# Kernel optimization log

Measured on AMD Instinct MI355X. Metric: run time of the kernel, lower is better.

The kernel has to match this reference:

```python
import jax, jax.numpy as jnp
import numpy as np

N, C, H, W = 4, 256, 60, 60
CIMG = 5  # rgb/ir channels after add_position (3 + x + y)
K = 8
ITERS = 2


def setup_inputs() -> dict:
    key = jax.random.key(0)
    ks = jax.random.split(key, 12)
    inp = {
        "cnn_encoder_output": jax.random.normal(ks[0], (N, C, H, W), jnp.float32),
        "rgb": jax.random.normal(ks[1], (N, CIMG, H, W), jnp.float32),
        "ir": jax.random.normal(ks[2], (N, CIMG, H, W), jnp.float32),
        # g-MLP (mlp_num_layers=1): Linear(2C -> C), torch weight layout [out, in]
        "W_g_rgb": jax.random.normal(ks[3], (C, 2 * C), jnp.float32) * 0.02,
        "b_g_rgb": jnp.zeros((C,), jnp.float32),
        "W_g_ir": jax.random.normal(ks[4], (C, 2 * C), jnp.float32) * 0.02,
        "b_g_ir": jnp.zeros((C,), jnp.float32),
        # SE block: Linear(2C -> C//16) -> ReLU -> Linear(C//16 -> C) -> Sigmoid
        "W_se1": jax.random.normal(ks[5], (C // 16, 2 * C), jnp.float32) * 0.02,
        "b_se1": jnp.zeros((C // 16,), jnp.float32),
        "W_se2": jax.random.normal(ks[6], (C, C // 16), jnp.float32) * 0.02,
        "b_se2": jnp.zeros((C,), jnp.float32),
        "gamma": jnp.ones((1,), jnp.float32),
        "gnn_iterations": ITERS,
        "k": K,
    }
    return inp


def _knn_indices(x, k):
    # x: [N, HW, D] -> indices of k nearest neighbours [N, HW, k]
    r = jnp.einsum("nid,njd->nij", x, x)          # gram matrix
    sq = jnp.einsum("nid,nid->ni", x, x)          # squared norms
    d2 = sq[:, :, None] + sq[:, None, :] - 2.0 * r
    d = jnp.sqrt(jnp.maximum(d2, 0.0))
    d = jax.lax.stop_gradient(d)
    _, idx = jax.lax.top_k(-d, k)                  # smallest distances
    return idx


def _gather(h, idx):
    # h: [N, HW, C], idx: [N, HW, K] -> [N, HW, K, C]
    return jax.vmap(lambda hn, i: hn[i])(h, idx)


def reference(cnn_encoder_output, rgb, ir, W_g_rgb, b_g_rgb, W_g_ir, b_g_ir,
              W_se1, b_se1, W_se2, b_se2, gamma, gnn_iterations, k):
    n, c, hh, ww = cnn_encoder_output.shape
    hw = hh * ww
    rgb_f = rgb.reshape(n, rgb.shape[1], hw).transpose(0, 2, 1)  # [N, HW, 5]
    ir_f = ir.reshape(n, ir.shape[1], hw).transpose(0, 2, 1)
    knn_rgb = _knn_indices(rgb_f, k)  # [N, HW, K]
    knn_ir = _knn_indices(ir_f, k)

    h = cnn_encoder_output.transpose(0, 2, 3, 1).reshape(n, hw, c)  # [N, HW, C]

    for _ in range(gnn_iterations):
        rgb_nb = _gather(h, knn_rgb)  # [N, HW, K, C]
        ir_nb = _gather(h, knn_ir)
        rgb_feat = jnp.concatenate([rgb_nb, rgb_nb - ir_nb], axis=-1)  # [N,HW,K,2C]
        ir_feat = jnp.concatenate([ir_nb, ir_nb - rgb_nb], axis=-1)
        m_rgb = jnp.max(jax.nn.relu(jnp.einsum("nhkf,cf->nhkc", rgb_feat, W_g_rgb) + b_g_rgb), axis=2)
        m_ir = jnp.max(jax.nn.relu(jnp.einsum("nhkf,cf->nhkc", ir_feat, W_g_ir) + b_g_ir), axis=2)
        cc = jnp.concatenate([m_rgb, m_ir], axis=-1).mean(axis=1, keepdims=True)  # [N,1,2C]
        se = jax.nn.sigmoid(jax.nn.relu(cc @ W_se1.T + b_se1) @ W_se2.T + b_se2)  # [N,1,C]
        h = se * h

    h = h.reshape(n, hh, ww, c).transpose(0, 3, 1, 2)
    return jax.nn.relu(gamma * h + cnn_encoder_output)
```

## Files before the change

kernel.cpp:

```cpp
#include <hip/hip_runtime.h>
#include <hip/hip_bf16.h>

#define NB 4
#define CH 256
#define HWT 3600
#define KNN 8
#define POSB 16
#define MPAD 3712

#define SSEGP 8
#define CAND 450
#define PAIRS 225
#define ROWS3 450

#define GEMM_BLKS 928

typedef __attribute__((ext_vector_type(8))) __bf16 bf16x8;
typedef __attribute__((ext_vector_type(4))) float f32x4;
typedef __attribute__((ext_vector_type(2))) float f32x2;
typedef __attribute__((ext_vector_type(2))) unsigned u32x2;
typedef __attribute__((ext_vector_type(4))) unsigned u32x4;

__device__ inline float med3f(float a, float b, float c) {
    return __builtin_amdgcn_fmed3f(a, b, c);
}

__device__ __forceinline__ void insert8(float* best, float kf) {
    best[7] = med3f(best[6], best[7], kf);
    best[6] = med3f(best[5], best[6], kf);
    best[5] = med3f(best[4], best[5], kf);
    best[4] = med3f(best[3], best[4], kf);
    best[3] = med3f(best[2], best[3], kf);
    best[2] = med3f(best[1], best[2], kf);
    best[1] = med3f(best[0], best[1], kf);
    best[0] = fminf(best[0], kf);
}


__device__ __forceinline__ void gemm_body(int lid, int n,
                                          const __hip_bfloat16* __restrict__ Abf,
                                          const __hip_bfloat16* __restrict__ Wbf,
                                          __hip_bfloat16* __restrict__ Yall,
                                          char* smem) {
    char* sA = smem;
    char* sB = smem + 16384;
    int w = (lid & 7) * 29 + (lid >> 3);
    int m0 = (w >> 3) * 128;
    int o0 = (w & 7) * 128;
    int t = threadIdx.x;
    int lane = t & 63, wid = t >> 6;
    int wm = wid >> 1, wo = wid & 1;

    const __hip_bfloat16* Ab = Abf + (size_t)n * MPAD * CH;
    const __hip_bfloat16* Wb = Wbf + (size_t)n * 1024 * CH;

    f32x4 acc[4][4] = {};

    int srow = t >> 3;
    int sslot = t & 7;
    int swz = (sslot ^ (srow & 7)) << 4;
    int fr = lane & 15;
    int kg = lane >> 4;
    int p = lane & 7;

    uint4 av[4], bv[4];
    auto load_tile = [&](int ks) {
#pragma unroll
        for (int r = 0; r < 4; ++r) {
            int row = srow + 32 * r;
            av[r] = *(const uint4*)(Ab + ((size_t)(m0 + row)) * CH + ks * 64 + sslot * 8);
            bv[r] = *(const uint4*)(Wb + ((size_t)(o0 + row)) * CH + ks * 64 + sslot * 8);
        }
    };
    load_tile(0);

    for (int ks = 0; ks < 4; ++ks) {
        __syncthreads();
#pragma unroll
        for (int r = 0; r < 4; ++r) {
            int row = srow + 32 * r;
            *(uint4*)(sA + row * 128 + swz) = av[r];
            *(uint4*)(sB + row * 128 + swz) = bv[r];
        }
        __syncthreads();
        if (ks < 3) load_tile(ks + 1);
#pragma unroll
        for (int kk = 0; kk < 2; ++kk) {
            bf16x8 hf[4], wf[4];
            int slot = kk * 4 + kg;
            int inrow = (slot ^ p) << 4;
#pragma unroll
            for (int f = 0; f < 4; ++f) {
                hf[f] = *(const bf16x8*)(sA + (wm * 64 + f * 16 + fr) * 128 + inrow);
                wf[f] = *(const bf16x8*)(sB + (wo * 64 + f * 16 + fr) * 128 + inrow);
            }
#pragma unroll
            for (int fa = 0; fa < 4; ++fa)
#pragma unroll
                for (int fb = 0; fb < 4; ++fb)
                    acc[fa][fb] = __builtin_amdgcn_mfma_f32_16x16x32_bf16(
                        wf[fa], hf[fb], acc[fa][fb], 0, 0, 0);
        }
    }

    __syncthreads();
#pragma unroll
    for (int fa = 0; fa < 4; ++fa)
#pragma unroll
        for (int fb = 0; fb < 4; ++fb) {
            int ml = wm * 64 + fb * 16 + fr;
            int ob = (wo * 64 + fa * 16 + kg * 4) * 2;
            f32x4 v = acc[fa][fb];
            union { ushort4 u; __hip_bfloat16 h[4]; } pk;
            pk.h[0] = __float2bfloat16(v.x);
            pk.h[1] = __float2bfloat16(v.y);
            pk.h[2] = __float2bfloat16(v.z);
            pk.h[3] = __float2bfloat16(v.w);
            int swzb = (ob & ~15) ^ ((ml & 15) << 4);
            *(ushort4*)(smem + ml * 256 + swzb + (ob & 15)) = pk.u;
        }
    __syncthreads();
    __hip_bfloat16* Y = Yall + (size_t)n * HWT * 1024;
    int colb = (t & 15) * 16;
#pragma unroll
    for (int i = 0; i < 8; ++i) {
        int row = i * 16 + (t >> 4);
        int grow = m0 + row;
        if (grow < HWT) {
            u32x4 v = *(const u32x4*)(smem + row * 256 + (colb ^ ((row & 15) << 4)));
            __builtin_nontemporal_store(v, (u32x4*)((char*)Y + (size_t)grow * 2048 + o0 * 2 + colb));
        }
    }
}

__global__ __launch_bounds__(256) void gemm_k(const __hip_bfloat16* __restrict__ Abf,
                                              const __hip_bfloat16* __restrict__ Wbf,
                                              __hip_bfloat16* __restrict__ Yall) {
    __shared__ char smem[32768];
    int gid = blockIdx.x;
    gemm_body(gid % 232, gid / 232, Abf, Wbf, Yall, smem);
}

__global__ __launch_bounds__(256) void knn_main(const float* __restrict__ xpack,
                                                unsigned* __restrict__ partial) {
    int seg = blockIdx.x, rb = blockIdx.y, nm = blockIdx.z;
    int t = threadIdx.x;
    const float* xp = xpack + (size_t)nm * HWT * 8;
    __shared__ f32x2 xs[PAIRS * 6];

    if (t < PAIRS) {
        int j = seg * CAND + 2 * t;
        float4 a0 = ((const float4*)xp)[(size_t)j * 2];
        float4 b0 = ((const float4*)xp)[(size_t)j * 2 + 1];
        float4 a1 = ((const float4*)xp)[(size_t)(j + 1) * 2];
        float4 b1 = ((const float4*)xp)[(size_t)(j + 1) * 2 + 1];
        f32x2* o = xs + t * 6;
        o[0] = f32x2{a0.x, a1.x};
        o[1] = f32x2{a0.y, a1.y};
        o[2] = f32x2{a0.z, a1.z};
        o[3] = f32x2{a0.w, a1.w};
        o[4] = f32x2{b0.x, b1.x};
        o[5] = f32x2{b0.y + 1.0f, b1.y + 1.0f};
    }
    __syncthreads();

    bool active = (t < PAIRS);
    int r0 = rb * ROWS3 + t;
    int rr0 = active ? r0 : 0;
    int rr1 = active ? (r0 + PAIRS) : 0;
    float4 a0 = ((const float4*)xp)[(size_t)rr0 * 2];
    float4 b0 = ((const float4*)xp)[(size_t)rr0 * 2 + 1];
    float4 a1 = ((const float4*)xp)[(size_t)rr1 * 2];
    float4 b1 = ((const float4*)xp)[(size_t)rr1 * 2 + 1];
    f32x2 q01 = f32x2{b0.y, b0.y};
    f32x2 q11 = f32x2{b1.y, b1.y};

    const float BIG = __uint_as_float(0x7F000000u);
    float bst0[8], bst1[8];
#pragma unroll
    for (int i = 0; i < 8; ++i) { bst0[i] = BIG; bst1[i] = BIG; }

    unsigned jg0 = (unsigned)(seg * CAND);
#pragma unroll 3
    for (int p = 0; p < PAIRS; ++p) {
        f32x2 cx = xs[p * 6 + 0];
        f32x2 cy = xs[p * 6 + 1];
        f32x2 cz = xs[p * 6 + 2];
        f32x2 cw = xs[p * 6 + 3];
        f32x2 cv = xs[p * 6 + 4];
        f32x2 cq = xs[p * 6 + 5];
        f32x2 d0 = cx * a0.x;
        d0 += cy * a0.y;
        d0 += cz * a0.z;
        d0 += cw * a0.w;
        d0 += cv * b0.x;
        f32x2 s0 = cq + q01;
        f32x2 e0 = s0 - 2.0f * d0;
        f32x2 d1 = cx * a1.x;
        d1 += cy * a1.y;
        d1 += cz * a1.z;
        d1 += cw * a1.w;
        d1 += cv * b1.x;
        f32x2 s1 = cq + q11;
        f32x2 e1 = s1 - 2.0f * d1;

        unsigned jA = jg0 + 2 * p, jB = jA + 1;
        u32x2 u0, u1;
        __builtin_memcpy(&u0, &e0, 8);
        __builtin_memcpy(&u1, &e1, 8);
        insert8(bst0, __uint_as_float((u0.x & 0xFFFFF000u) | jA));
        insert8(bst0, __uint_as_float((u0.y & 0xFFFFF000u) | jB));
        insert8(bst1, __uint_as_float((u1.x & 0xFFFFF000u) | jA));
        insert8(bst1, __uint_as_float((u1.y & 0xFFFFF000u) | jB));
    }
    if (active) {
        unsigned* o = partial + (((size_t)(nm * SSEGP + seg)) * HWT + r0) * 8;
        ((uint4*)o)[0] = uint4{ __float_as_uint(bst0[0]), __float_as_uint(bst0[1]),
                                __float_as_uint(bst0[2]), __float_as_uint(bst0[3]) };
        ((uint4*)o)[1] = uint4{ __float_as_uint(bst0[4]), __float_as_uint(bst0[5]),
                                __float_as_uint(bst0[6]), __float_as_uint(bst0[7]) };
        unsigned* o1 = partial + (((size_t)(nm * SSEGP + seg)) * HWT + r0 + PAIRS) * 8;
        ((uint4*)o1)[0] = uint4{ __float_as_uint(bst1[0]), __float_as_uint(bst1[1]),
                                 __float_as_uint(bst1[2]), __float_as_uint(bst1[3]) };
        ((uint4*)o1)[1] = uint4{ __float_as_uint(bst1[4]), __float_as_uint(bst1[5]),
                                 __float_as_uint(bst1[6]), __float_as_uint(bst1[7]) };
    }
}

__global__ __launch_bounds__(256) void fusedA(const float* __restrict__ cnn,
                                              __hip_bfloat16* __restrict__ Abf,
                                              const float* __restrict__ Wg_rgb,
                                              const float* __restrict__ Wg_ir,
                                              float* __restrict__ Wcomb,
                                              float* __restrict__ g,
                                              __hip_bfloat16* __restrict__ Wbf,
                                              const float* __restrict__ rgb,
                                              const float* __restrict__ ir,
                                              float* __restrict__ xpack) {
    int bid = blockIdx.x;
    int t = threadIdx.x;
    if (bid < GEMM_BLKS) {
        __shared__ float st[64][65];
        int n = bid / 232;
        int rem = bid - n * 232;
        int k0 = (rem / 58) * 64;
        int m0 = (rem % 58) * 64;
        const float* src = cnn + (size_t)n * CH * HWT;
#pragma unroll
        for (int r = 0; r < 4; ++r) {
            int kl = r * 16 + (t >> 4);
            int ms = (t & 15) * 4;
            float4 v = {0.f, 0.f, 0.f, 0.f};
            if (m0 + ms < HWT) v = *(const float4*)(src + (size_t)(k0 + kl) * HWT + m0 + ms);
            st[ms + 0][kl] = v.x; st[ms + 1][kl] = v.y;
            st[ms + 2][kl] = v.z; st[ms + 3][kl] = v.w;
        }
        __syncthreads();
        int m = t >> 2, kg = (t & 3) * 16;
        union { uint4 u[2]; __hip_bfloat16 h[16]; } pk;
#pragma unroll
        for (int i = 0; i < 16; ++i) pk.h[i] = __float2bfloat16(st[m][kg + i]);
        __hip_bfloat16* dst = Abf + ((size_t)n * MPAD + m0 + m) * CH + k0 + kg;
        ((uint4*)dst)[0] = pk.u[0];
        ((uint4*)dst)[1] = pk.u[1];
    } else if (bid < GEMM_BLKS + 1024) {
        int e = (bid - GEMM_BLKS) * 256 + t;
        int o = e >> 8, j = e & 255;
        float v;
        if (o < 256)      v = Wg_rgb[o * 512 + j] + Wg_rgb[o * 512 + 256 + j];
        else if (o < 512) v = Wg_rgb[(o - 256) * 512 + 256 + j];
        else if (o < 768) v = Wg_ir[(o - 512) * 512 + j] + Wg_ir[(o - 512) * 512 + 256 + j];
        else              v = Wg_ir[(o - 768) * 512 + 256 + j];
        Wcomb[e] = v;
        __hip_bfloat16 h = __float2bfloat16(v);
#pragma unroll
        for (int n = 0; n < NB; ++n) Wbf[(size_t)n * 262144 + e] = h;
        if (e < NB * CH) g[e] = 1.0f;
    } else {
        int e = (bid - GEMM_BLKS - 1024) * 256 + t;
        if (e < 2 * NB * HWT) {
            int nm = e / HWT, j = e - nm * HWT;
            int mod = nm / NB, n = nm - mod * NB;
            const float* x = (mod == 0 ? rgb : ir) + (size_t)n * 5 * HWT;
            float v[5], q = 0.f;
#pragma unroll
            for (int d = 0; d < 5; ++d) { v[d] = x[d * HWT + j]; q = fmaf(v[d], v[d], q); }
            float* o = xpack + (size_t)e * 8;
#pragma unroll
            for (int d = 0; d < 5; ++d) o[d] = v[d];
            o[5] = q; o[6] = 0.f; o[7] = 0.f;
        }
    }
}

__global__ __launch_bounds__(256) void knn_merge_zero(const unsigned* __restrict__ partial,
                                                      int* __restrict__ knn_rgb,
                                                      int* __restrict__ knn_ir,
                                                      float* __restrict__ ccsum) {
    int bid = blockIdx.x;
    if (bid >= 450) {
        int e = (bid - 450) * 256 + threadIdx.x;
        if (e < NB * 512) ccsum[e] = 0.f;
        return;
    }
    int tid = bid * 256 + threadIdx.x;
    int rid = tid >> 1, sub = tid & 1;
    int nm = rid / HWT, row = rid - nm * HWT;
    const float BIG = __uint_as_float(0x7F000000u);
    float best[8];
#pragma unroll
    for (int i = 0; i < 8; ++i) best[i] = BIG;
    for (int s = sub; s < SSEGP; s += 2) {
        const unsigned* p = partial + (((size_t)(nm * SSEGP + s)) * HWT + row) * 8;
#pragma unroll
        for (int w = 0; w < 2; ++w) {
            uint4 v = ((const uint4*)p)[w];
            unsigned vv[4] = { v.x, v.y, v.z, v.w };
#pragma unroll
            for (int e = 0; e < 4; ++e) insert8(best, __uint_as_float(vv[e]));
        }
    }
    float other[8];
#pragma unroll
    for (int i = 0; i < 8; ++i) other[i] = __shfl_xor(best[i], 1);
#pragma unroll
    for (int i = 0; i < 8; ++i) insert8(best, other[i]);
    if (sub == 0) {
        int mod = nm / NB, n = nm - mod * NB;
        int* o = (mod == 0 ? knn_rgb : knn_ir) + ((size_t)n * HWT + row) * KNN;
#pragma unroll
        for (int i = 0; i < 8; ++i) o[i] = (int)(__float_as_uint(best[i]) & 0xFFFu);
    }
}

__global__ __launch_bounds__(256) void scale_w_zero(const float* __restrict__ Wcomb,
                                                    const float* __restrict__ g,
                                                    __hip_bfloat16* __restrict__ Wbf,
                                                    float* __restrict__ ccsum) {
    int bid = blockIdx.x;
    if (bid >= 512) {
        int e = (bid - 512) * 256 + threadIdx.x;
        if (e < NB * 512) ccsum[e] = 0.f;
        return;
    }
    int n = bid >> 7;
    int gid = (bid & 127) * 256 + threadIdx.x;
    int o = gid >> 5;
    int kb = (gid & 31) * 8;
    const float* w = Wcomb + o * 256 + kb;
    const float* gp = g + n * CH + kb;
    union { uint4 u; __hip_bfloat16 h[8]; } pk;
#pragma unroll
    for (int i = 0; i < 8; ++i) pk.h[i] = __float2bfloat16(w[i] * gp[i]);
    *(uint4*)(Wbf + ((size_t)n * 1024 + o) * CH + kb) = pk.u;
}

__global__ __launch_bounds__(256) void gather_kernel(const __hip_bfloat16* __restrict__ Yall,
                                                     const int* __restrict__ knn_rgb,
                                                     const int* __restrict__ knn_ir,
                                                     const float* __restrict__ b_rgb,
                                                     const float* __restrict__ b_ir,
                                                     float* __restrict__ ccsum) {
    int lid = blockIdx.x;
    int xcd = lid & 7, sub = lid >> 3;
    int wg = (xcd < 4 ? xcd * 113 : 4 * 113 + (xcd - 4) * 112) + sub;
    int n = wg / 225;
    int hwbase = (wg - n * 225) * POSB;
    int t = threadIdx.x;
    int half = t >> 7;
    int cp = (t & 127) << 1;
    __shared__ int sidx[POSB][2][KNN];
    {
        int p = t >> 4, rem = t & 15;
        int hw = hwbase + p;
        int v;
        if (rem < 8) v = knn_rgb[((size_t)n * HWT + hw) * KNN + rem];
        else         v = knn_ir[((size_t)n * HWT + hw) * KNN + (rem - 8)];
        sidx[p][rem >> 3][rem & 7] = v;
    }
    __syncthreads();
    const float* bias = half ? b_ir : b_rgb;
    float b0 = bias[cp], b1 = bias[cp + 1];
    float acc0 = 0.f, acc1 = 0.f;
    const __hip_bfloat16* Y = Yall + (size_t)n * HWT * 1024;
    int offA = half * 512 + cp;
    int offB = half * 512 + 256 + cp;
    for (int p = 0; p < POSB; ++p) {
        float m0 = 0.f, m1 = 0.f;
#pragma unroll
        for (int k = 0; k < KNN; ++k) {
            int jA = sidx[p][half][k];
            int jB = sidx[p][half ^ 1][k];
            unsigned u1 = *(const unsigned*)(Y + (size_t)jA * 1024 + offA);
            unsigned u2 = *(const unsigned*)(Y + (size_t)jB * 1024 + offB);
            float a0 = __uint_as_float(u1 << 16);
            float a1 = __uint_as_float(u1 & 0xFFFF0000u);
            float c0 = __uint_as_float(u2 << 16);
            float c1 = __uint_as_float(u2 & 0xFFFF0000u);
            m0 = fmaxf(m0, a0 - c0 + b0);
            m1 = fmaxf(m1, a1 - c1 + b1);
        }
        acc0 += m0;
        acc1 += m1;
    }
    atomicAdd(&ccsum[n * 512 + half * 256 + cp], acc0);
    atomicAdd(&ccsum[n * 512 + half * 256 + cp + 1], acc1);
}

__global__ __launch_bounds__(256) void se_kernel(const float* __restrict__ ccsum,
                                                 const float* __restrict__ W1,
                                                 const float* __restrict__ b1,
                                                 const float* __restrict__ W2,
                                                 const float* __restrict__ b2,
                                                 float* __restrict__ g) {
    int n = blockIdx.x;
    int t = threadIdx.x;
    __shared__ float hid[16];
    __shared__ float cc[512];
    cc[t] = ccsum[n * 512 + t] * (1.0f / HWT);
    cc[256 + t] = ccsum[n * 512 + 256 + t] * (1.0f / HWT);
    __syncthreads();
    if (t < 16) {
        float s = b1[t];
        for (int j = 0; j < 512; ++j) s = fmaf(W1[t * 512 + j], cc[j], s);
        hid[t] = fmaxf(s, 0.f);
    }
    __syncthreads();
    float s = b2[t];
#pragma unroll
    for (int q = 0; q < 16; ++q) s = fmaf(W2[t * 16 + q], hid[q], s);
    float se = 1.0f / (1.0f + expf(-s));
    g[n * CH + t] *= se;
}

__global__ void final_kernel(const float* __restrict__ cnn, const float* __restrict__ g,
                             const float* __restrict__ gamma, float* __restrict__ out) {
    int t = blockIdx.x * blockDim.x + threadIdx.x;
    if (t >= NB * CH * HWT / 4) return;
    int nc = (t * 4) / HWT;
    float4 x = ((const float4*)cnn)[t];
    float s = gamma[0] * g[nc] + 1.0f;
    float4 o;
    o.x = fmaxf(s * x.x, 0.f);
    o.y = fmaxf(s * x.y, 0.f);
    o.z = fmaxf(s * x.z, 0.f);
    o.w = fmaxf(s * x.w, 0.f);
    ((float4*)out)[t] = o;
}

extern "C" void kernel_launch(void* const* d_in, const int* in_sizes, int n_in,
                              void* d_out, int out_size, void* d_ws, size_t ws_size,
                              hipStream_t stream) {
    const float* cnn    = (const float*)d_in[0];
    const float* rgb    = (const float*)d_in[1];
    const float* ir     = (const float*)d_in[2];
    const float* Wg_rgb = (const float*)d_in[3];
    const float* bg_rgb = (const float*)d_in[4];
    const float* Wg_ir  = (const float*)d_in[5];
    const float* bg_ir  = (const float*)d_in[6];
    const float* Wse1   = (const float*)d_in[7];
    const float* bse1   = (const float*)d_in[8];
    const float* Wse2   = (const float*)d_in[9];
    const float* bse2   = (const float*)d_in[10];
    const float* gamma  = (const float*)d_in[11];
    float* out = (float*)d_out;

    char* ws = (char*)d_ws;
    size_t off = 0;
    float* xpack = (float*)(ws + off); off += (size_t)2 * NB * HWT * 8 * 4;
    int* knn_rgb = (int*)(ws + off); off += (size_t)NB * HWT * KNN * 4;
    int* knn_ir  = (int*)(ws + off); off += (size_t)NB * HWT * KNN * 4;
    float* Wcomb = (float*)(ws + off); off += (size_t)1024 * 256 * 4;
    __hip_bfloat16* Wbf = (__hip_bfloat16*)(ws + off); off += (size_t)NB * 1024 * CH * 2;
    __hip_bfloat16* Abf = (__hip_bfloat16*)(ws + off); off += (size_t)NB * MPAD * CH * 2;
    __hip_bfloat16* Yall = (__hip_bfloat16*)(ws + off); off += (size_t)NB * HWT * 1024 * 2;
    unsigned* partial = (unsigned*)(ws + off);
    off += (size_t)2 * NB * SSEGP * HWT * 8 * 4;
    float* ccsum = (float*)(ws + off); off += (size_t)NB * 512 * 4;
    float* g     = (float*)(ws + off); off += (size_t)NB * CH * 4;

    fusedA<<<GEMM_BLKS + 1024 + 113, 256, 0, stream>>>(cnn, Abf, Wg_rgb, Wg_ir, Wcomb, g,
                                                       Wbf, rgb, ir, xpack);
    knn_main<<<dim3(SSEGP, 8, 2 * NB), 256, 0, stream>>>(xpack, partial);
    gemm_k<<<GEMM_BLKS, 256, 0, stream>>>(Abf, Wbf, Yall);
    knn_merge_zero<<<458, 256, 0, stream>>>(partial, knn_rgb, knn_ir, ccsum);
    gather_kernel<<<900, 256, 0, stream>>>(Yall, knn_rgb, knn_ir, bg_rgb, bg_ir, ccsum);
    se_kernel<<<NB, 256, 0, stream>>>(ccsum, Wse1, bse1, Wse2, bse2, g);
    scale_w_zero<<<520, 256, 0, stream>>>(Wcomb, g, Wbf, ccsum);
    gemm_k<<<GEMM_BLKS, 256, 0, stream>>>(Abf, Wbf, Yall);
    gather_kernel<<<900, 256, 0, stream>>>(Yall, knn_rgb, knn_ir, bg_rgb, bg_ir, ccsum);
    se_kernel<<<NB, 256, 0, stream>>>(ccsum, Wse1, bse1, Wse2, bse2, g);
    final_kernel<<<3600, 256, 0, stream>>>(cnn, g, gamma, out);
}
```

Before: 239.4 us.

## Split kNN candidates into more segments and use scalar distance loop

```diff
diff --git a/kernel.cpp b/kernel.cpp
--- a/kernel.cpp
+++ b/kernel.cpp
@@ -8,17 +8,14 @@
 #define POSB 16
 #define MPAD 3712
 
-#define SSEGP 8
-#define CAND 450
-#define PAIRS 225
-#define ROWS3 450
+#define SSEGP 16
+#define CAND 225
+#define RB 8
 
 #define GEMM_BLKS 928
 
 typedef __attribute__((ext_vector_type(8))) __bf16 bf16x8;
 typedef __attribute__((ext_vector_type(4))) float f32x4;
-typedef __attribute__((ext_vector_type(2))) float f32x2;
-typedef __attribute__((ext_vector_type(2))) unsigned u32x2;
 typedef __attribute__((ext_vector_type(4))) unsigned u32x4;
 
 __device__ inline float med3f(float a, float b, float c) {
@@ -146,72 +143,54 @@
     int seg = blockIdx.x, rb = blockIdx.y, nm = blockIdx.z;
     int t = threadIdx.x;
     const float* xp = xpack + (size_t)nm * HWT * 8;
-    __shared__ f32x2 xs[PAIRS * 6];
-
-    if (t < PAIRS) {
-        int j = seg * CAND + 2 * t;
-        float4 a0 = ((const float4*)xp)[(size_t)j * 2];
-        float4 b0 = ((const float4*)xp)[(size_t)j * 2 + 1];
-        float4 a1 = ((const float4*)xp)[(size_t)(j + 1) * 2];
-        float4 b1 = ((const float4*)xp)[(size_t)(j + 1) * 2 + 1];
-        f32x2* o = xs + t * 6;
-        o[0] = f32x2{a0.x, a1.x};
-        o[1] = f32x2{a0.y, a1.y};
-        o[2] = f32x2{a0.z, a1.z};
-        o[3] = f32x2{a0.w, a1.w};
-        o[4] = f32x2{b0.x, b1.x};
-        o[5] = f32x2{b0.y + 1.0f, b1.y + 1.0f};
-    }
-    __syncthreads();
-
-    bool active = (t < PAIRS);
-    int r0 = rb * ROWS3 + t;
+    __shared__ float4 xs4[CAND];
+    __shared__ float2 xs2[CAND];
+    int j0 = seg * CAND;
+    if (t < CAND) {
+        float4 a = ((const float4*)xp)[(size_t)(j0 + t) * 2];
+        float4 b = ((const float4*)xp)[(size_t)(j0 + t) * 2 + 1];
+        xs4[t] = a;
+        xs2[t] = float2{b.x, b.y + 1.0f};
+    }
+    __syncthreads();
+
+    bool active = (t < CAND);
+    int r0 = rb * 450 + t;
     int rr0 = active ? r0 : 0;
-    int rr1 = active ? (r0 + PAIRS) : 0;
+    int rr1 = active ? (r0 + CAND) : 0;
     float4 a0 = ((const float4*)xp)[(size_t)rr0 * 2];
     float4 b0 = ((const float4*)xp)[(size_t)rr0 * 2 + 1];
     float4 a1 = ((const float4*)xp)[(size_t)rr1 * 2];
     float4 b1 = ((const float4*)xp)[(size_t)rr1 * 2 + 1];
-    f32x2 q01 = f32x2{b0.y, b0.y};
-    f32x2 q11 = f32x2{b1.y, b1.y};
+    float q0 = b0.y, q1 = b1.y;
 
     const float BIG = __uint_as_float(0x7F000000u);
     float bst0[8], bst1[8];
 #pragma unroll
     for (int i = 0; i < 8; ++i) { bst0[i] = BIG; bst1[i] = BIG; }
 
-    unsigned jg0 = (unsigned)(seg * CAND);
-#pragma unroll 3
-    for (int p = 0; p < PAIRS; ++p) {
-        f32x2 cx = xs[p * 6 + 0];
-        f32x2 cy = xs[p * 6 + 1];
-        f32x2 cz = xs[p * 6 + 2];
-        f32x2 cw = xs[p * 6 + 3];
-        f32x2 cv = xs[p * 6 + 4];
-        f32x2 cq = xs[p * 6 + 5];
-        f32x2 d0 = cx * a0.x;
-        d0 += cy * a0.y;
-        d0 += cz * a0.z;
-        d0 += cw * a0.w;
-        d0 += cv * b0.x;
-        f32x2 s0 = cq + q01;
-        f32x2 e0 = s0 - 2.0f * d0;
-        f32x2 d1 = cx * a1.x;
-        d1 += cy * a1.y;
-        d1 += cz * a1.z;
-        d1 += cw * a1.w;
-        d1 += cv * b1.x;
-        f32x2 s1 = cq + q11;
-        f32x2 e1 = s1 - 2.0f * d1;
-
-        unsigned jA = jg0 + 2 * p, jB = jA + 1;
-        u32x2 u0, u1;
-        __builtin_memcpy(&u0, &e0, 8);
-        __builtin_memcpy(&u1, &e1, 8);
-        insert8(bst0, __uint_as_float((u0.x & 0xFFFFF000u) | jA));
-        insert8(bst0, __uint_as_float((u0.y & 0xFFFFF000u) | jB));
-        insert8(bst1, __uint_as_float((u1.x & 0xFFFFF000u) | jA));
-        insert8(bst1, __uint_as_float((u1.y & 0xFFFFF000u) | jB));
+    unsigned jg0 = (unsigned)j0;
+#pragma unroll 5
+    for (int jj = 0; jj < CAND; ++jj) {
+        float4 a = xs4[jj];
+        float2 b = xs2[jj];
+        unsigned jg = jg0 + jj;
+        float d0 = a.x * a0.x;
+        d0 = fmaf(a.y, a0.y, d0);
+        d0 = fmaf(a.z, a0.z, d0);
+        d0 = fmaf(a.w, a0.w, d0);
+        d0 = fmaf(b.x, b0.x, d0);
+        float e0 = fmaf(-2.0f, d0, b.y + q0);
+        float d1 = a.x * a1.x;
+        d1 = fmaf(a.y, a1.y, d1);
+        d1 = fmaf(a.z, a1.z, d1);
+        d1 = fmaf(a.w, a1.w, d1);
+        d1 = fmaf(b.x, b1.x, d1);
+        float e1 = fmaf(-2.0f, d1, b.y + q1);
+        float k0 = __uint_as_float((__float_as_uint(e0) & 0xFFFFF000u) | jg);
+        float k1 = __uint_as_float((__float_as_uint(e1) & 0xFFFFF000u) | jg);
+        insert8(bst0, k0);
+        insert8(bst1, k1);
     }
     if (active) {
         unsigned* o = partial + (((size_t)(nm * SSEGP + seg)) * HWT + r0) * 8;
@@ -219,7 +198,7 @@
                                 __float_as_uint(bst0[2]), __float_as_uint(bst0[3]) };
         ((uint4*)o)[1] = uint4{ __float_as_uint(bst0[4]), __float_as_uint(bst0[5]),
                                 __float_as_uint(bst0[6]), __float_as_uint(bst0[7]) };
-        unsigned* o1 = partial + (((size_t)(nm * SSEGP + seg)) * HWT + r0 + PAIRS) * 8;
+        unsigned* o1 = partial + (((size_t)(nm * SSEGP + seg)) * HWT + r0 + CAND) * 8;
         ((uint4*)o1)[0] = uint4{ __float_as_uint(bst1[0]), __float_as_uint(bst1[1]),
                                  __float_as_uint(bst1[2]), __float_as_uint(bst1[3]) };
         ((uint4*)o1)[1] = uint4{ __float_as_uint(bst1[4]), __float_as_uint(bst1[5]),
@@ -481,7 +460,7 @@
 
     fusedA<<<GEMM_BLKS + 1024 + 113, 256, 0, stream>>>(cnn, Abf, Wg_rgb, Wg_ir, Wcomb, g,
                                                        Wbf, rgb, ir, xpack);
-    knn_main<<<dim3(SSEGP, 8, 2 * NB), 256, 0, stream>>>(xpack, partial);
+    knn_main<<<dim3(SSEGP, RB, 2 * NB), 256, 0, stream>>>(xpack, partial);
     gemm_k<<<GEMM_BLKS, 256, 0, stream>>>(Abf, Wbf, Yall);
     knn_merge_zero<<<458, 256, 0, stream>>>(partial, knn_rgb, knn_ir, ccsum);
     gather_kernel<<<900, 256, 0, stream>>>(Yall, knn_rgb, knn_ir, bg_rgb, bg_ir, ccsum);
```

New measurement: 226.4 us. 1.06x faster.
